# Optimization experiments

Hardware: AMD Instinct MI355X
Metric: run time of the kernel (lower is better)

The kernel has to match this reference:

```python
import jax, jax.numpy as jnp
import numpy as np

BN_EPS = 1e-5
ATT_EPS = 1e-6


def _conv(x, w, groups=1):
    # x: [B,C,H,W], w: [O, C//groups, k, k], stride 1, SAME padding for odd k
    k = w.shape[-1]
    p = (k - 1) // 2
    return jax.lax.conv_general_dilated(
        x, w, window_strides=(1, 1), padding=[(p, p), (p, p)],
        dimension_numbers=('NCHW', 'OIHW', 'NCHW'), feature_group_count=groups)


def _bn(x, bnp):
    # bnp: [4, C] stacked (scale, bias, running_mean, running_var); eval-mode BN
    s, b, m, v = bnp[0], bnp[1], bnp[2], bnp[3]
    inv = s / jnp.sqrt(v + BN_EPS)
    return x * inv[None, :, None, None] + (b - m * inv)[None, :, None, None]


def _relu6(x):
    return jnp.clip(x, 0.0, 6.0)


def _ffn(x, fc1_w, fc1_bn, conv1_w, conv1_bn, conv2_w, conv2_bn, fc2_w, fc2_bn):
    # E_FFN: 1x1 ConvBNReLU6 -> dw5x5 ConvBNReLU6 & dw3x3 ConvBNReLU6 -> sum -> 1x1 ConvBN -> ReLU6
    C = x.shape[1]
    h = _relu6(_bn(_conv(x, fc1_w), fc1_bn))
    x1 = _relu6(_bn(_conv(h, conv1_w, groups=C), conv1_bn))
    x2 = _relu6(_bn(_conv(h, conv2_w, groups=C), conv2_bn))
    return _relu6(_bn(_conv(x1 + x2, fc2_w), fc2_bn))


def _bias(y, b):
    return y + b[None, :, None, None]


def setup_inputs() -> dict:
    key = jax.random.key(0)
    ks = jax.random.split(key, 16)
    C, M = 64, 8  # in_places, in_places // scale
    B, H, W = 4, 224, 224

    def w(k, shape, s=0.05):
        return (jax.random.normal(k, shape, dtype=jnp.float32) * s)

    def bn_params(k, c):
        k1, k2, k3, k4 = jax.random.split(k, 4)
        scale = 1.0 + 0.1 * jax.random.normal(k1, (c,), dtype=jnp.float32)
        bias = 0.1 * jax.random.normal(k2, (c,), dtype=jnp.float32)
        mean = 0.1 * jax.random.normal(k3, (c,), dtype=jnp.float32)
        var = 1.0 + 0.1 * jax.random.uniform(k4, (c,), dtype=jnp.float32)
        return jnp.stack([scale, bias, mean, var])  # [4, c]

    return {
        'x': jax.random.normal(ks[0], (B, C, H, W), dtype=jnp.float32),
        'gamma': jnp.full((1,), 0.5, dtype=jnp.float32),  # nonzero so attention branch matters
        'q_w': w(ks[1], (M, C, 1, 1)), 'q_b': w(ks[2], (M,)),
        'k_w': w(ks[3], (M, C, 1, 1)), 'k_b': w(ks[4], (M,)),
        'v_w': w(ks[5], (C, C, 1, 1)), 'v_b': w(ks[6], (C,)),
        'fc1_w': w(ks[7], (C, C, 1, 1)), 'fc1_bn': bn_params(ks[8], C),
        'conv1_w': w(ks[9], (C, 1, 5, 5)), 'conv1_bn': bn_params(ks[10], C),
        'conv2_w': w(ks[11], (C, 1, 3, 3)), 'conv2_bn': bn_params(ks[12], C),
        'fc2_w': w(ks[13], (C, C, 1, 1)), 'fc2_bn': bn_params(ks[14], C),
    }


def reference(x, gamma, q_w, q_b, k_w, k_b, v_w, v_b,
              fc1_w, fc1_bn, conv1_w, conv1_bn, conv2_w, conv2_bn, fc2_w, fc2_bn):
    B, C, H, W = x.shape
    N = H * W
    x_channel = _ffn(x, fc1_w, fc1_bn, conv1_w, conv1_bn, conv2_w, conv2_bn, fc2_w, fc2_bn)
    # softplus feature maps; Q,K: [B, m, N]
    Q = jax.nn.softplus(_bias(_conv(x, q_w), q_b).reshape(B, -1, N))
    K = jax.nn.softplus(_bias(_conv(x, k_w), k_b).reshape(B, -1, N))
    V = (_bias(_conv(x, v_w), v_b) + x_channel).reshape(B, C, N)
    Qt = jnp.swapaxes(Q, 1, 2)                              # [B, N, m]
    KV = jnp.einsum('bmn,bcn->bmc', K, V)                   # [B, m, C]
    norm = 1.0 / jnp.einsum('bnm,bm->bn', Qt, K.sum(-1) + ATT_EPS)  # [B, N]
    wv = jnp.einsum('bnm,bmc,bn->bcn', Qt, KV, norm).reshape(B, C, H, W)
    return x + gamma * wv
```

## Files before the change

### kernel.cpp

```cpp
#include <hip/hip_runtime.h>
#include <math.h>

#define B_ 4
#define C_ 64
#define M_ 8
#define H_ 224
#define W_ 224
#define N_ (H_*W_)
#define CN_ (C_*N_)
#define MN_ (M_*N_)
#define BCN_ (B_*CN_)
#define BMN_ (B_*MN_)

__device__ __forceinline__ float relu6f(float v){ return fminf(fmaxf(v,0.0f),6.0f); }
__device__ __forceinline__ float softplusf(float v){
  return v > 0.0f ? v + log1pf(expf(-v)) : log1pf(expf(v));
}

__global__ __launch_bounds__(256) void k_fc1k(const float* __restrict__ x,
                                              const float* __restrict__ w,
                                              const float* __restrict__ bn,
                                              const float* __restrict__ kw,
                                              const float* __restrict__ kb,
                                              float* __restrict__ h,
                                              float* __restrict__ Kq)
{
  __shared__ __align__(16) float wt[64*32];
  __shared__ __align__(16) float kt[64*8];
  const int tid  = threadIdx.x;
  const int b    = blockIdx.x / 392;
  const int rem  = blockIdx.x % 392;
  const int pg   = rem >> 1;
  const int half = rem & 1;

  for (int idx = tid; idx < 2048; idx += 256) {
    const int c = idx >> 5, o = idx & 31;
    wt[idx] = w[(half*32 + o)*64 + c];
  }
  for (int idx = tid; idx < 512; idx += 256) {
    const int c = idx >> 3, m = idx & 7;
    kt[idx] = kw[m*64 + c];
  }
  __syncthreads();

  const int lane = tid & 63, wave = tid >> 6;
  const int pix = pg*256 + 4*lane;
  const float* xb = x + (size_t)b*CN_ + pix;
  const int obl = wave*8;
  const int ob  = half*32 + obl;

  float4 acc[8];
  float4 ak0 = {0,0,0,0}, ak1 = {0,0,0,0};
  #pragma unroll
  for (int i = 0; i < 8; ++i) acc[i] = make_float4(0.f,0.f,0.f,0.f);

  float4 xv = *(const float4*)xb;
  #pragma unroll 4
  for (int c = 0; c < 64; ++c) {
    const size_t nxt = (c < 63) ? (size_t)(c+1)*N_ : (size_t)63*N_;
    const float4 xn = *(const float4*)(xb + nxt);
    const float4 w0 = *(const float4*)&wt[c*32 + obl];
    const float4 w1 = *(const float4*)&wt[c*32 + obl + 4];
    const float2 k2 = *(const float2*)&kt[c*8 + wave*2];
    const float wv[8] = {w0.x,w0.y,w0.z,w0.w,w1.x,w1.y,w1.z,w1.w};
    #pragma unroll
    for (int o = 0; o < 8; ++o) {
      acc[o].x = fmaf(wv[o], xv.x, acc[o].x);
      acc[o].y = fmaf(wv[o], xv.y, acc[o].y);
      acc[o].z = fmaf(wv[o], xv.z, acc[o].z);
      acc[o].w = fmaf(wv[o], xv.w, acc[o].w);
    }
    if (half == 0) {
      ak0.x = fmaf(k2.x, xv.x, ak0.x); ak0.y = fmaf(k2.x, xv.y, ak0.y);
      ak0.z = fmaf(k2.x, xv.z, ak0.z); ak0.w = fmaf(k2.x, xv.w, ak0.w);
      ak1.x = fmaf(k2.y, xv.x, ak1.x); ak1.y = fmaf(k2.y, xv.y, ak1.y);
      ak1.z = fmaf(k2.y, xv.z, ak1.z); ak1.w = fmaf(k2.y, xv.w, ak1.w);
    }
    xv = xn;
  }

  float* hb = h + (size_t)b*CN_ + pix;
  #pragma unroll
  for (int o = 0; o < 8; ++o) {
    const int oc = ob + o;
    const float inv  = bn[oc] / sqrtf(bn[192+oc] + 1e-5f);
    const float beta = bn[64+oc] - bn[128+oc]*inv;
    float4 o4;
    o4.x = relu6f(fmaf(acc[o].x, inv, beta));
    o4.y = relu6f(fmaf(acc[o].y, inv, beta));
    o4.z = relu6f(fmaf(acc[o].z, inv, beta));
    o4.w = relu6f(fmaf(acc[o].w, inv, beta));
    *(float4*)(hb + (size_t)oc*N_) = o4;
  }
  if (half == 0) {
    const int m0 = wave*2;
    const float kb0 = kb[m0], kb1 = kb[m0+1];
    float* Kb = Kq + (size_t)b*MN_ + pix;
    float4 q0, q1;
    q0.x = softplusf(ak0.x+kb0); q0.y = softplusf(ak0.y+kb0);
    q0.z = softplusf(ak0.z+kb0); q0.w = softplusf(ak0.w+kb0);
    q1.x = softplusf(ak1.x+kb1); q1.y = softplusf(ak1.y+kb1);
    q1.z = softplusf(ak1.z+kb1); q1.w = softplusf(ak1.w+kb1);
    *(float4*)(Kb + (size_t)m0*N_)     = q0;
    *(float4*)(Kb + (size_t)(m0+1)*N_) = q1;
  }
}

__global__ __launch_bounds__(256) void k_dw(const float* __restrict__ h,
                                            const float* __restrict__ w5,
                                            const float* __restrict__ w3,
                                            const float* __restrict__ bn1,
                                            const float* __restrict__ bn2,
                                            float* __restrict__ s)
{
  __shared__ float tile[36*37];
  const int tid = threadIdx.x;
  const int blk = blockIdx.x;
  const int t   = blk % 49;
  const int bc  = blk / 49;
  const int c   = bc & 63;
  const int tx0 = (t % 7) * 32;
  const int ty0 = (t / 7) * 32;
  const float* hb = h + (size_t)bc * N_;

  for (int idx = tid; idx < 1296; idx += 256) {
    const int ly = idx / 36, lx = idx - ly*36;
    const int gy = ty0 + ly - 2, gx = tx0 + lx - 2;
    float v = 0.0f;
    if (gy >= 0 && gy < H_ && gx >= 0 && gx < W_) v = hb[gy*W_ + gx];
    tile[ly*37 + lx] = v;
  }
  __syncthreads();

  float w5r[25], w3r[9];
  #pragma unroll
  for (int i = 0; i < 25; ++i) w5r[i] = w5[c*25 + i];
  #pragma unroll
  for (int i = 0; i < 9; ++i)  w3r[i] = w3[c*9 + i];
  const float inv1 = bn1[c] / sqrtf(bn1[192+c] + 1e-5f);
  const float bet1 = bn1[64+c] - bn1[128+c]*inv1;
  const float inv2 = bn2[c] / sqrtf(bn2[192+c] + 1e-5f);
  const float bet2 = bn2[64+c] - bn2[128+c]*inv2;

  const int ty  = tid >> 3;
  const int tx4 = (tid & 7) << 2;
  float a5[4] = {0,0,0,0}, a3[4] = {0,0,0,0};
  #pragma unroll
  for (int dy = 0; dy < 5; ++dy) {
    float r[8];
    #pragma unroll
    for (int i = 0; i < 8; ++i) r[i] = tile[(ty+dy)*37 + tx4 + i];
    #pragma unroll
    for (int dx = 0; dx < 5; ++dx) {
      const float wv = w5r[dy*5+dx];
      #pragma unroll
      for (int p = 0; p < 4; ++p) a5[p] = fmaf(wv, r[p+dx], a5[p]);
    }
    if (dy >= 1 && dy <= 3) {
      #pragma unroll
      for (int dx = 1; dx <= 3; ++dx) {
        const float wv = w3r[(dy-1)*3+(dx-1)];
        #pragma unroll
        for (int p = 0; p < 4; ++p) a3[p] = fmaf(wv, r[p+dx], a3[p]);
      }
    }
  }
  float* sb = s + (size_t)bc * N_ + (ty0+ty)*W_ + tx0 + tx4;
  float4 o4;
  o4.x = relu6f(fmaf(a5[0],inv1,bet1)) + relu6f(fmaf(a3[0],inv2,bet2));
  o4.y = relu6f(fmaf(a5[1],inv1,bet1)) + relu6f(fmaf(a3[1],inv2,bet2));
  o4.z = relu6f(fmaf(a5[2],inv1,bet1)) + relu6f(fmaf(a3[2],inv2,bet2));
  o4.w = relu6f(fmaf(a5[3],inv1,bet1)) + relu6f(fmaf(a3[3],inv2,bet2));
  *(float4*)sb = o4;
}

__global__ __launch_bounds__(256) void k_v(const float* __restrict__ x,
                                           const float* __restrict__ s,
                                           const float* __restrict__ vw,
                                           const float* __restrict__ vb,
                                           const float* __restrict__ fw,
                                           const float* __restrict__ fbn,
                                           float* __restrict__ V)
{
  __shared__ __align__(16) float wtv[64*32];
  __shared__ __align__(16) float wtf[64*32];
  const int tid  = threadIdx.x;
  const int b    = blockIdx.x / 392;
  const int rem  = blockIdx.x % 392;
  const int pg   = rem >> 1;
  const int half = rem & 1;

  for (int idx = tid; idx < 2048; idx += 256) {
    const int c = idx >> 5, o = idx & 31;
    wtv[idx] = vw[(half*32 + o)*64 + c];
    wtf[idx] = fw[(half*32 + o)*64 + c];
  }
  __syncthreads();

  const int lane = tid & 63, wave = tid >> 6;
  const int pix = pg*256 + 4*lane;
  const float* xb = x + (size_t)b*CN_ + pix;
  const float* sb = s + (size_t)b*CN_ + pix;
  const int obl = wave*8;
  const int ob  = half*32 + obl;

  float4 av[8], af[8];
  #pragma unroll
  for (int i = 0; i < 8; ++i) { av[i] = make_float4(0,0,0,0); af[i] = make_float4(0,0,0,0); }

  float4 xv = *(const float4*)xb;
  float4 sv = *(const float4*)sb;
  #pragma unroll 4
  for (int c = 0; c < 64; ++c) {
    const size_t nxt = (c < 63) ? (size_t)(c+1)*N_ : (size_t)63*N_;
    const float4 xn = *(const float4*)(xb + nxt);
    const float4 sn = *(const float4*)(sb + nxt);
    const float4 a0 = *(const float4*)&wtv[c*32 + obl];
    const float4 a1 = *(const float4*)&wtv[c*32 + obl + 4];
    const float4 f0 = *(const float4*)&wtf[c*32 + obl];
    const float4 f1 = *(const float4*)&wtf[c*32 + obl + 4];
    const float wa[8] = {a0.x,a0.y,a0.z,a0.w,a1.x,a1.y,a1.z,a1.w};
    const float wf[8] = {f0.x,f0.y,f0.z,f0.w,f1.x,f1.y,f1.z,f1.w};
    #pragma unroll
    for (int o = 0; o < 8; ++o) {
      av[o].x = fmaf(wa[o], xv.x, av[o].x);
      av[o].y = fmaf(wa[o], xv.y, av[o].y);
      av[o].z = fmaf(wa[o], xv.z, av[o].z);
      av[o].w = fmaf(wa[o], xv.w, av[o].w);
      af[o].x = fmaf(wf[o], sv.x, af[o].x);
      af[o].y = fmaf(wf[o], sv.y, af[o].y);
      af[o].z = fmaf(wf[o], sv.z, af[o].z);
      af[o].w = fmaf(wf[o], sv.w, af[o].w);
    }
    xv = xn; sv = sn;
  }

  float* Vb = V + (size_t)b*CN_ + pix;
  #pragma unroll
  for (int o = 0; o < 8; ++o) {
    const int oc = ob + o;
    const float inv  = fbn[oc] / sqrtf(fbn[192+oc] + 1e-5f);
    const float beta = fbn[64+oc] - fbn[128+oc]*inv;
    const float bias = vb[oc];
    float4 o4;
    o4.x = av[o].x + bias + relu6f(fmaf(af[o].x, inv, beta));
    o4.y = av[o].y + bias + relu6f(fmaf(af[o].y, inv, beta));
    o4.z = av[o].z + bias + relu6f(fmaf(af[o].z, inv, beta));
    o4.w = av[o].w + bias + relu6f(fmaf(af[o].w, inv, beta));
    *(float4*)(Vb + (size_t)oc*N_) = o4;
  }
}

__global__ __launch_bounds__(256) void k_kv(const float* __restrict__ V,
                                            const float* __restrict__ Kq,
                                            float* __restrict__ KV,
                                            float* __restrict__ Ksum)
{
  const int blk = blockIdx.x;
  const int b   = blk >> 7;
  const int rem = blk & 127;
  const int cg  = rem >> 4;
  const int ch  = rem & 15;
  const int tid = threadIdx.x;
  const int base = ch * 3136;
  const int end  = base + 3136;
  const float* Kb = Kq + (size_t)b*MN_;
  const float* Vb = V  + (size_t)b*CN_ + (size_t)(cg*8)*N_;

  float acc[64];
  #pragma unroll
  for (int i = 0; i < 64; ++i) acc[i] = 0.0f;
  float ks[8] = {0,0,0,0,0,0,0,0};

  for (int n = base + tid; n < end; n += 256) {
    float kv[8];
    #pragma unroll
    for (int m2 = 0; m2 < 8; ++m2) kv[m2] = Kb[m2*N_ + n];
    #pragma unroll
    for (int m2 = 0; m2 < 8; ++m2) ks[m2] += kv[m2];
    #pragma unroll
    for (int c8 = 0; c8 < 8; ++c8) {
      const float vv = Vb[c8*N_ + n];
      #pragma unroll
      for (int m2 = 0; m2 < 8; ++m2)
        acc[m2*8+c8] = fmaf(kv[m2], vv, acc[m2*8+c8]);
    }
  }
  const int lane = tid & 63;
  float mine = 0.0f;
  #pragma unroll
  for (int jj = 0; jj < 64; ++jj) {
    float v = acc[jj];
    v += __shfl_xor(v, 1);
    v += __shfl_xor(v, 2);
    v += __shfl_xor(v, 4);
    v += __shfl_xor(v, 8);
    v += __shfl_xor(v, 16);
    v += __shfl_xor(v, 32);
    if (lane == jj) mine = v;
  }
  atomicAdd(&KV[b*512 + (lane>>3)*64 + cg*8 + (lane&7)], mine);
  if (cg == 0) {
    float mk = 0.0f;
    #pragma unroll
    for (int jj = 0; jj < 8; ++jj) {
      float v = ks[jj];
      v += __shfl_xor(v, 1);
      v += __shfl_xor(v, 2);
      v += __shfl_xor(v, 4);
      v += __shfl_xor(v, 8);
      v += __shfl_xor(v, 16);
      v += __shfl_xor(v, 32);
      if (lane == jj) mk = v;
    }
    if (lane < 8) atomicAdd(&Ksum[b*8 + lane], mk);
  }
}

__global__ __launch_bounds__(256) void k_out(const float* __restrict__ x,
                                             const float* __restrict__ qw,
                                             const float* __restrict__ qb,
                                             const float* __restrict__ gamma,
                                             const float* __restrict__ KV,
                                             const float* __restrict__ Ksum,
                                             float* __restrict__ out)
{
  __shared__ float xs[64*256];
  __shared__ __align__(16) float kvt[64*8];
  __shared__ __align__(16) float wqt[64*8];
  __shared__ float ksl[8];
  const int tid = threadIdx.x;
  const int b  = blockIdx.x / 196;
  const int pg = blockIdx.x % 196;
  const int pix0 = pg*256;
  const float* xb = x + (size_t)b*CN_ + pix0;

  for (int idx = tid; idx < 512; idx += 256) {
    const int m = idx >> 6, c = idx & 63;
    kvt[c*8 + m] = KV[b*512 + idx];
    wqt[c*8 + m] = qw[idx];
  }
  if (tid < 8) ksl[tid] = Ksum[b*8 + tid] + 1e-6f;
  for (int idx = tid; idx < 4096; idx += 256) {
    const int c = idx >> 6, i = idx & 63;
    const float4 v = ((const float4*)(xb + (size_t)c*N_))[i];
    ((float4*)&xs[c*256])[i] = v;
  }
  __syncthreads();

  float q[8] = {0,0,0,0,0,0,0,0};
  #pragma unroll 8
  for (int c = 0; c < 64; ++c) {
    const float xv = xs[c*256 + tid];
    const float4 w0 = *(const float4*)&wqt[c*8];
    const float4 w1 = *(const float4*)&wqt[c*8+4];
    q[0] = fmaf(w0.x, xv, q[0]);
    q[1] = fmaf(w0.y, xv, q[1]);
    q[2] = fmaf(w0.z, xv, q[2]);
    q[3] = fmaf(w0.w, xv, q[3]);
    q[4] = fmaf(w1.x, xv, q[4]);
    q[5] = fmaf(w1.y, xv, q[5]);
    q[6] = fmaf(w1.z, xv, q[6]);
    q[7] = fmaf(w1.w, xv, q[7]);
  }
  float den = 0.0f;
  #pragma unroll
  for (int m = 0; m < 8; ++m) {
    q[m] = softplusf(q[m] + qb[m]);
    den  = fmaf(q[m], ksl[m], den);
  }
  const float sc = gamma[0] / den;

  float* ob = out + (size_t)b*CN_ + pix0 + tid;
  #pragma unroll 8
  for (int c = 0; c < 64; ++c) {
    const float4 k0 = *(const float4*)&kvt[c*8];
    const float4 k1 = *(const float4*)&kvt[c*8+4];
    float wv;
    wv = q[0]*k0.x;
    wv = fmaf(q[1], k0.y, wv);
    wv = fmaf(q[2], k0.z, wv);
    wv = fmaf(q[3], k0.w, wv);
    wv = fmaf(q[4], k1.x, wv);
    wv = fmaf(q[5], k1.y, wv);
    wv = fmaf(q[6], k1.z, wv);
    wv = fmaf(q[7], k1.w, wv);
    ob[(size_t)c*N_] = fmaf(sc, wv, xs[c*256 + tid]);
  }
}

extern "C" void kernel_launch(void* const* d_in, const int* in_sizes, int n_in,
                              void* d_out, int out_size, void* d_ws, size_t ws_size,
                              hipStream_t stream) {
  const float* x      = (const float*)d_in[0];
  const float* gamma  = (const float*)d_in[1];
  const float* q_w    = (const float*)d_in[2];
  const float* q_b    = (const float*)d_in[3];
  const float* k_w    = (const float*)d_in[4];
  const float* k_b    = (const float*)d_in[5];
  const float* v_w    = (const float*)d_in[6];
  const float* v_b    = (const float*)d_in[7];
  const float* fc1_w  = (const float*)d_in[8];
  const float* fc1_bn = (const float*)d_in[9];
  const float* c1_w   = (const float*)d_in[10];
  const float* c1_bn  = (const float*)d_in[11];
  const float* c2_w   = (const float*)d_in[12];
  const float* c2_bn  = (const float*)d_in[13];
  const float* fc2_w  = (const float*)d_in[14];
  const float* fc2_bn = (const float*)d_in[15];
  float* outp = (float*)d_out;

  float* ws   = (float*)d_ws;
  float* bufA = ws;
  float* bufS = ws + (size_t)BCN_;
  float* bufK = ws + (size_t)2*BCN_;
  float* kv   = ws + (size_t)2*BCN_ + BMN_;
  float* ksum = kv + 2048;

  hipMemsetAsync(kv, 0, (2048 + 32)*sizeof(float), stream);

  k_fc1k<<<dim3(B_*392), dim3(256), 0, stream>>>(x, fc1_w, fc1_bn, k_w, k_b, bufA, bufK);
  k_dw  <<<dim3(B_*C_*49), dim3(256), 0, stream>>>(bufA, c1_w, c2_w, c1_bn, c2_bn, bufS);
  k_v   <<<dim3(B_*392), dim3(256), 0, stream>>>(x, bufS, v_w, v_b, fc2_w, fc2_bn, bufA);
  k_kv  <<<dim3(512), dim3(256), 0, stream>>>(bufA, bufK, kv, ksum);
  k_out <<<dim3(B_*196), dim3(256), 0, stream>>>(x, q_w, q_b, gamma, kv, ksum, outp);
}
```

Before: 365.6 us.

## Stage input channel chunks in double-buffered LDS for 1x1 conv kernels

The fc1/K and V/fc2 pointwise-conv kernels now load 8-channel chunks of the input pixels and weights into double-buffered shared memory. Each block covers 128 pixels for all 64 output channels, so x and s are read from global memory once per block rather than once per half of the output channels. The K projection is spread across all waves instead of being handled only by half==0 blocks. This adds LDS traffic and a barrier per chunk, and the smaller pixel tile per block lowers the number of pixels each block processes.

```diff
diff --git a/kernel.cpp b/kernel.cpp
--- a/kernel.cpp
+++ b/kernel.cpp
@@ -17,6 +17,9 @@
   return v > 0.0f ? v + log1pf(expf(-v)) : log1pf(expf(v));
 }
 
+#define FMA4(A, W, X) { A.x = fmaf((W), (X).x, A.x); A.y = fmaf((W), (X).y, A.y); \
+                        A.z = fmaf((W), (X).z, A.z); A.w = fmaf((W), (X).w, A.w); }
+
 __global__ __launch_bounds__(256) void k_fc1k(const float* __restrict__ x,
                                               const float* __restrict__ w,
                                               const float* __restrict__ bn,
@@ -25,84 +28,94 @@
                                               float* __restrict__ h,
                                               float* __restrict__ Kq)
 {
-  __shared__ __align__(16) float wt[64*32];
-  __shared__ __align__(16) float kt[64*8];
+  __shared__ float xsl[2*1024];
+  __shared__ float wl [2*512];
+  __shared__ float kt [512];
   const int tid  = threadIdx.x;
   const int b    = blockIdx.x / 392;
-  const int rem  = blockIdx.x % 392;
-  const int pg   = rem >> 1;
-  const int half = rem & 1;
-
-  for (int idx = tid; idx < 2048; idx += 256) {
-    const int c = idx >> 5, o = idx & 31;
-    wt[idx] = w[(half*32 + o)*64 + c];
-  }
+  const int pg   = blockIdx.x % 392;
+  const int pix0 = pg*128;
+  const float* xb = x + (size_t)b*CN_ + pix0;
+
   for (int idx = tid; idx < 512; idx += 256) {
     const int c = idx >> 3, m = idx & 7;
     kt[idx] = kw[m*64 + c];
   }
+
+  const int scp = tid >> 5;
+  const int spx = (tid & 31) << 2;
+  const int e0 = tid*2, e1 = tid*2+1;
+  const int wc0 = e0 >> 6, wo0 = e0 & 63;
+  const int wc1 = e1 >> 6, wo1 = e1 & 63;
+
+  {
+    const float4 xr = *(const float4*)(xb + (size_t)scp*N_ + spx);
+    const float w0r = w[wo0*64 + wc0];
+    const float w1r = w[wo1*64 + wc1];
+    *(float4*)&xsl[scp*128 + spx] = xr;
+    wl[e0] = w0r; wl[e1] = w1r;
+  }
   __syncthreads();
 
-  const int lane = tid & 63, wave = tid >> 6;
-  const int pix = pg*256 + 4*lane;
-  const float* xb = x + (size_t)b*CN_ + pix;
-  const int obl = wave*8;
-  const int ob  = half*32 + obl;
-
-  float4 acc[8];
-  float4 ak0 = {0,0,0,0}, ak1 = {0,0,0,0};
-  #pragma unroll
-  for (int i = 0; i < 8; ++i) acc[i] = make_float4(0.f,0.f,0.f,0.f);
-
-  float4 xv = *(const float4*)xb;
-  #pragma unroll 4
-  for (int c = 0; c < 64; ++c) {
-    const size_t nxt = (c < 63) ? (size_t)(c+1)*N_ : (size_t)63*N_;
-    const float4 xn = *(const float4*)(xb + nxt);
-    const float4 w0 = *(const float4*)&wt[c*32 + obl];
-    const float4 w1 = *(const float4*)&wt[c*32 + obl + 4];
-    const float2 k2 = *(const float2*)&kt[c*8 + wave*2];
-    const float wv[8] = {w0.x,w0.y,w0.z,w0.w,w1.x,w1.y,w1.z,w1.w};
-    #pragma unroll
-    for (int o = 0; o < 8; ++o) {
-      acc[o].x = fmaf(wv[o], xv.x, acc[o].x);
-      acc[o].y = fmaf(wv[o], xv.y, acc[o].y);
-      acc[o].z = fmaf(wv[o], xv.z, acc[o].z);
-      acc[o].w = fmaf(wv[o], xv.w, acc[o].w);
-    }
-    if (half == 0) {
-      ak0.x = fmaf(k2.x, xv.x, ak0.x); ak0.y = fmaf(k2.x, xv.y, ak0.y);
-      ak0.z = fmaf(k2.x, xv.z, ak0.z); ak0.w = fmaf(k2.x, xv.w, ak0.w);
-      ak1.x = fmaf(k2.y, xv.x, ak1.x); ak1.y = fmaf(k2.y, xv.y, ak1.y);
-      ak1.z = fmaf(k2.y, xv.z, ak1.z); ak1.w = fmaf(k2.y, xv.w, ak1.w);
-    }
-    xv = xn;
-  }
-
-  float* hb = h + (size_t)b*CN_ + pix;
+  const int lane = tid & 63, wv_ = tid >> 6;
+  const int och  = 2*wv_ + (lane >> 5);
+  const int ocb  = och*8;
+  const int px4  = (lane & 31) << 2;
+
+  float4 ah[8];
+  float4 ak = {0,0,0,0};
+  #pragma unroll
+  for (int i = 0; i < 8; ++i) ah[i] = make_float4(0.f,0.f,0.f,0.f);
+
+  for (int ck = 0; ck < 8; ++ck) {
+    const int cur = ck & 1, nxt = cur ^ 1;
+    const float* xc = &xsl[cur*1024];
+    const float* wc = &wl[cur*512];
+    float4 xr; float w0r, w1r;
+    if (ck < 7) {
+      const int c0n = (ck+1)*8;
+      xr  = *(const float4*)(xb + (size_t)(c0n + scp)*N_ + spx);
+      w0r = w[wo0*64 + c0n + wc0];
+      w1r = w[wo1*64 + c0n + wc1];
+    }
+    #pragma unroll
+    for (int cp = 0; cp < 8; ++cp) {
+      const float4 xv = *(const float4*)&xc[cp*128 + px4];
+      const float4 w0 = *(const float4*)&wc[cp*64 + ocb];
+      const float4 w1 = *(const float4*)&wc[cp*64 + ocb + 4];
+      const float kvw = kt[(ck*8+cp)*8 + och];
+      FMA4(ah[0], w0.x, xv); FMA4(ah[1], w0.y, xv);
+      FMA4(ah[2], w0.z, xv); FMA4(ah[3], w0.w, xv);
+      FMA4(ah[4], w1.x, xv); FMA4(ah[5], w1.y, xv);
+      FMA4(ah[6], w1.z, xv); FMA4(ah[7], w1.w, xv);
+      FMA4(ak, kvw, xv);
+    }
+    if (ck < 7) {
+      *(float4*)&xsl[nxt*1024 + scp*128 + spx] = xr;
+      wl[nxt*512 + e0] = w0r; wl[nxt*512 + e1] = w1r;
+    }
+    __syncthreads();
+  }
+
+  float* hb = h + (size_t)b*CN_ + pix0 + px4;
   #pragma unroll
   for (int o = 0; o < 8; ++o) {
-    const int oc = ob + o;
+    const int oc = ocb + o;
     const float inv  = bn[oc] / sqrtf(bn[192+oc] + 1e-5f);
     const float beta = bn[64+oc] - bn[128+oc]*inv;
     float4 o4;
-    o4.x = relu6f(fmaf(acc[o].x, inv, beta));
-    o4.y = relu6f(fmaf(acc[o].y, inv, beta));
-    o4.z = relu6f(fmaf(acc[o].z, inv, beta));
-    o4.w = relu6f(fmaf(acc[o].w, inv, beta));
+    o4.x = relu6f(fmaf(ah[o].x, inv, beta));
+    o4.y = relu6f(fmaf(ah[o].y, inv, beta));
+    o4.z = relu6f(fmaf(ah[o].z, inv, beta));
+    o4.w = relu6f(fmaf(ah[o].w, inv, beta));
     *(float4*)(hb + (size_t)oc*N_) = o4;
   }
-  if (half == 0) {
-    const int m0 = wave*2;
-    const float kb0 = kb[m0], kb1 = kb[m0+1];
-    float* Kb = Kq + (size_t)b*MN_ + pix;
-    float4 q0, q1;
-    q0.x = softplusf(ak0.x+kb0); q0.y = softplusf(ak0.y+kb0);
-    q0.z = softplusf(ak0.z+kb0); q0.w = softplusf(ak0.w+kb0);
-    q1.x = softplusf(ak1.x+kb1); q1.y = softplusf(ak1.y+kb1);
-    q1.z = softplusf(ak1.z+kb1); q1.w = softplusf(ak1.w+kb1);
-    *(float4*)(Kb + (size_t)m0*N_)     = q0;
-    *(float4*)(Kb + (size_t)(m0+1)*N_) = q1;
+  {
+    const float kbm = kb[och];
+    float4 q;
+    q.x = softplusf(ak.x + kbm); q.y = softplusf(ak.y + kbm);
+    q.z = softplusf(ak.z + kbm); q.w = softplusf(ak.w + kbm);
+    *(float4*)(Kq + (size_t)b*MN_ + (size_t)och*N_ + pix0 + px4) = q;
   }
 }
 
@@ -182,63 +195,88 @@
                                            const float* __restrict__ fbn,
                                            float* __restrict__ V)
 {
-  __shared__ __align__(16) float wtv[64*32];
-  __shared__ __align__(16) float wtf[64*32];
+  __shared__ float xsl[2*1024];
+  __shared__ float ssl[2*1024];
+  __shared__ float wvl[2*512];
+  __shared__ float wfl[2*512];
   const int tid  = threadIdx.x;
   const int b    = blockIdx.x / 392;
-  const int rem  = blockIdx.x % 392;
-  const int pg   = rem >> 1;
-  const int half = rem & 1;
-
-  for (int idx = tid; idx < 2048; idx += 256) {
-    const int c = idx >> 5, o = idx & 31;
-    wtv[idx] = vw[(half*32 + o)*64 + c];
-    wtf[idx] = fw[(half*32 + o)*64 + c];
+  const int pg   = blockIdx.x % 392;
+  const int pix0 = pg*128;
+  const float* xb = x + (size_t)b*CN_ + pix0;
+  const float* sb = s + (size_t)b*CN_ + pix0;
+
+  const int scp = tid >> 5;
+  const int spx = (tid & 31) << 2;
+  const int e0 = tid*2, e1 = tid*2+1;
+  const int wc0 = e0 >> 6, wo0 = e0 & 63;
+  const int wc1 = e1 >> 6, wo1 = e1 & 63;
+
+  {
+    const float4 xr = *(const float4*)(xb + (size_t)scp*N_ + spx);
+    const float4 sr = *(const float4*)(sb + (size_t)scp*N_ + spx);
+    const float a0 = vw[wo0*64 + wc0], a1 = vw[wo1*64 + wc1];
+    const float f0 = fw[wo0*64 + wc0], f1 = fw[wo1*64 + wc1];
+    *(float4*)&xsl[scp*128 + spx] = xr;
+    *(float4*)&ssl[scp*128 + spx] = sr;
+    wvl[e0] = a0; wvl[e1] = a1;
+    wfl[e0] = f0; wfl[e1] = f1;
   }
   __syncthreads();
 
-  const int lane = tid & 63, wave = tid >> 6;
-  const int pix = pg*256 + 4*lane;
-  const float* xb = x + (size_t)b*CN_ + pix;
-  const float* sb = s + (size_t)b*CN_ + pix;
-  const int obl = wave*8;
-  const int ob  = half*32 + obl;
+  const int lane = tid & 63, wv_ = tid >> 6;
+  const int och  = 2*wv_ + (lane >> 5);
+  const int ocb  = och*8;
+  const int px4  = (lane & 31) << 2;
 
   float4 av[8], af[8];
   #pragma unroll
   for (int i = 0; i < 8; ++i) { av[i] = make_float4(0,0,0,0); af[i] = make_float4(0,0,0,0); }
 
-  float4 xv = *(const float4*)xb;
-  float4 sv = *(const float4*)sb;
-  #pragma unroll 4
-  for (int c = 0; c < 64; ++c) {
-    const size_t nxt = (c < 63) ? (size_t)(c+1)*N_ : (size_t)63*N_;
-    const float4 xn = *(const float4*)(xb + nxt);
-    const float4 sn = *(const float4*)(sb + nxt);
-    const float4 a0 = *(const float4*)&wtv[c*32 + obl];
-    const float4 a1 = *(const float4*)&wtv[c*32 + obl + 4];
-    const float4 f0 = *(const float4*)&wtf[c*32 + obl];
-    const float4 f1 = *(const float4*)&wtf[c*32 + obl + 4];
-    const float wa[8] = {a0.x,a0.y,a0.z,a0.w,a1.x,a1.y,a1.z,a1.w};
-    const float wf[8] = {f0.x,f0.y,f0.z,f0.w,f1.x,f1.y,f1.z,f1.w};
-    #pragma unroll
-    for (int o = 0; o < 8; ++o) {
-      av[o].x = fmaf(wa[o], xv.x, av[o].x);
-      av[o].y = fmaf(wa[o], xv.y, av[o].y);
-      av[o].z = fmaf(wa[o], xv.z, av[o].z);
-      av[o].w = fmaf(wa[o], xv.w, av[o].w);
-      af[o].x = fmaf(wf[o], sv.x, af[o].x);
-      af[o].y = fmaf(wf[o], sv.y, af[o].y);
-      af[o].z = fmaf(wf[o], sv.z, af[o].z);
-      af[o].w = fmaf(wf[o], sv.w, af[o].w);
-    }
-    xv = xn; sv = sn;
-  }
-
-  float* Vb = V + (size_t)b*CN_ + pix;
+  for (int ck = 0; ck < 8; ++ck) {
+    const int cur = ck & 1, nxt = cur ^ 1;
+    const float* xc = &xsl[cur*1024];
+    const float* sc2 = &ssl[cur*1024];
+    const float* wvc = &wvl[cur*512];
+    const float* wfc = &wfl[cur*512];
+    float4 xr, sr; float a0r, a1r, f0r, f1r;
+    if (ck < 7) {
+      const int c0n = (ck+1)*8;
+      xr  = *(const float4*)(xb + (size_t)(c0n + scp)*N_ + spx);
+      sr  = *(const float4*)(sb + (size_t)(c0n + scp)*N_ + spx);
+      a0r = vw[wo0*64 + c0n + wc0]; a1r = vw[wo1*64 + c0n + wc1];
+      f0r = fw[wo0*64 + c0n + wc0]; f1r = fw[wo1*64 + c0n + wc1];
+    }
+    #pragma unroll
+    for (int cp = 0; cp < 8; ++cp) {
+      const float4 xv = *(const float4*)&xc[cp*128 + px4];
+      const float4 sv = *(const float4*)&sc2[cp*128 + px4];
+      const float4 wa0 = *(const float4*)&wvc[cp*64 + ocb];
+      const float4 wa1 = *(const float4*)&wvc[cp*64 + ocb + 4];
+      const float4 wf0 = *(const float4*)&wfc[cp*64 + ocb];
+      const float4 wf1 = *(const float4*)&wfc[cp*64 + ocb + 4];
+      FMA4(av[0], wa0.x, xv); FMA4(av[1], wa0.y, xv);
+      FMA4(av[2], wa0.z, xv); FMA4(av[3], wa0.w, xv);
+      FMA4(av[4], wa1.x, xv); FMA4(av[5], wa1.y, xv);
+      FMA4(av[6], wa1.z, xv); FMA4(av[7], wa1.w, xv);
+      FMA4(af[0], wf0.x, sv); FMA4(af[1], wf0.y, sv);
+      FMA4(af[2], wf0.z, sv); FMA4(af[3], wf0.w, sv);
+      FMA4(af[4], wf1.x, sv); FMA4(af[5], wf1.y, sv);
+      FMA4(af[6], wf1.z, sv); FMA4(af[7], wf1.w, sv);
+    }
+    if (ck < 7) {
+      *(float4*)&xsl[nxt*1024 + scp*128 + spx] = xr;
+      *(float4*)&ssl[nxt*1024 + scp*128 + spx] = sr;
+      wvl[nxt*512 + e0] = a0r; wvl[nxt*512 + e1] = a1r;
+      wfl[nxt*512 + e0] = f0r; wfl[nxt*512 + e1] = f1r;
+    }
+    __syncthreads();
+  }
+
+  float* Vb = V + (size_t)b*CN_ + pix0 + px4;
   #pragma unroll
   for (int o = 0; o < 8; ++o) {
-    const int oc = ob + o;
+    const int oc = ocb + o;
     const float inv  = fbn[oc] / sqrtf(fbn[192+oc] + 1e-5f);
     const float beta = fbn[64+oc] - fbn[128+oc]*inv;
     const float bias = vb[oc];
```

Result: faster. 308.6 us (-15.6%).
